# Optimization experiments

Measured on AMD Instinct MI355X. Metric: run time of the kernel, lower is better.

## Reference

```python
import jax, jax.numpy as jnp
import numpy as np

N_CTX = 4096
D_MODEL = 2048
D_HEAD = 128


def setup_inputs() -> dict:
    key = jax.random.key(0)
    k1, k2, k3, k4 = jax.random.split(key, 4)
    x = jax.random.normal(k1, (N_CTX, D_MODEL), dtype=jnp.float32)
    # torch nn.Linear weights are [out, in]; kept in that layout.
    Wk = jax.random.normal(k2, (D_HEAD, D_MODEL), dtype=jnp.float32) * (1.0 / np.sqrt(D_MODEL))
    Wq = jax.random.normal(k3, (D_HEAD, D_MODEL), dtype=jnp.float32) * (1.0 / np.sqrt(D_MODEL))
    W2 = jax.random.normal(k4, (D_MODEL, D_MODEL), dtype=jnp.float32) * (1.0 / np.sqrt(D_MODEL))
    return {"x": x, "Wk": Wk, "Wq": Wq, "W2": W2}


def reference(x, Wk, Wq, W2):
    # Faithful to the torch module: no 1/sqrt(d_head) scaling, V = x itself.
    n = x.shape[0]
    q = x @ Wq.T                     # [n, d_head]
    k = x @ Wk.T                     # [n, d_head]
    scores = q @ k.T                 # [n, n]
    # causal mask: strictly-upper-triangular entries -> -inf
    causal = jnp.tril(jnp.ones((n, n), dtype=bool))
    scores = jnp.where(causal, scores, -jnp.inf)
    attn = jax.nn.softmax(scores, axis=1)  # [n, n]
    out = attn @ x                   # [n, d_model] (V is the raw input)
    return out @ W2.T                # [n, d_model]
```

## Files before the change

### kernel.cpp

```cpp
#include <hip/hip_runtime.h>

#define NCTX 4096
#define DMODEL 2048
#define DHEAD 128

typedef _Float16 f16;
typedef f16 f16x8 __attribute__((ext_vector_type(8)));
typedef float f32x4 __attribute__((ext_vector_type(4)));
typedef unsigned short u16;

__device__ __forceinline__ u16 f2h(float f) {
  union { f16 h; u16 u; } v; v.h = (f16)f; return v.u;
}
__device__ __forceinline__ float h2f(u16 u) {
  union { u16 u; f16 h; } v; v.u = u; return (float)v.h;
}

__device__ __forceinline__ void gl_lds16(const void* g, void* l) {
  __builtin_amdgcn_global_load_lds((const __attribute__((address_space(1))) void*)g,
                                   (__attribute__((address_space(3))) void*)l, 16, 0, 0);
}

__device__ __forceinline__ void splitH4(float4 v, ushort4& h, ushort4& l) {
  h.x = f2h(v.x); l.x = f2h(v.x - h2f(h.x));
  h.y = f2h(v.y); l.y = f2h(v.y - h2f(h.y));
  h.z = f2h(v.z); l.z = f2h(v.z - h2f(h.z));
  h.w = f2h(v.w); l.w = f2h(v.w - h2f(h.w));
}

__global__ __launch_bounds__(256) void prep_all(const float* __restrict__ x,
                                                const float* __restrict__ Wq,
                                                const float* __restrict__ Wk,
                                                const float* __restrict__ W2,
                                                u16* __restrict__ xh, u16* __restrict__ xl,
                                                u16* __restrict__ Wf, u16* __restrict__ W2f,
                                                u16* __restrict__ XT) {
  __shared__ float tile[64][65];
  int b = blockIdx.x;
  int t = threadIdx.x;
  if (b < 2048) {
    int mb = (b >> 5) * 64, db = (b & 31) * 64;
    int tx = t & 15, ty = t >> 4;
#pragma unroll
    for (int rr = 0; rr < 4; ++rr) {
      int row = rr * 16 + ty;
      float4 v = *(const float4*)(x + (size_t)(mb + row) * DMODEL + db + tx * 4);
      ushort4 h, l; splitH4(v, h, l);
      size_t gi = ((size_t)(mb + row) * DMODEL + db) / 4 + tx;
      ((ushort4*)xh)[gi] = h; ((ushort4*)xl)[gi] = l;
      tile[row][tx * 4 + 0] = v.x; tile[row][tx * 4 + 1] = v.y;
      tile[row][tx * 4 + 2] = v.z; tile[row][tx * 4 + 3] = v.w;
    }
    __syncthreads();
#pragma unroll
    for (int rr = 0; rr < 4; ++rr) {
      int r = (t >> 4) * 4 + rr;
      int c0 = (t & 15) * 4;
      ushort4 o;
      o.x = f2h(tile[c0 + 0][r]); o.y = f2h(tile[c0 + 1][r]);
      o.z = f2h(tile[c0 + 2][r]); o.w = f2h(tile[c0 + 3][r]);
      *(ushort4*)(XT + (size_t)(db + r) * NCTX + mb + c0) = o;
    }
  } else if (b < 2560) {
    int wk = (b >= 2304);
    int i = (b - (wk ? 2304 : 2048)) * 256 + t;
    const float* W = wk ? Wk : Wq;
    size_t off = wk ? ((size_t)DHEAD * DMODEL / 4) : 0;
    float4 v = ((const float4*)W)[i];
    ushort4 o;
    o.x = f2h(v.x); o.y = f2h(v.y); o.z = f2h(v.z); o.w = f2h(v.w);
    ((ushort4*)Wf)[off + i] = o;
  } else {
    int i = (b - 2560) * 256 + t;
    float4 v = ((const float4*)W2)[i];
    ushort4 o;
    o.x = f2h(v.x); o.y = f2h(v.y); o.z = f2h(v.z); o.w = f2h(v.w);
    ((ushort4*)W2f)[i] = o;
  }
}

__global__ __launch_bounds__(256) void reduce8_f16(const float* __restrict__ P,
                                                   u16* __restrict__ out, int n4) {
  int i = blockIdx.x * 256 + threadIdx.x;
  if (i >= n4) return;
  float4 s = ((const float4*)P)[i];
#pragma unroll
  for (int z = 1; z < 8; ++z) {
    float4 v = ((const float4*)P)[(size_t)z * n4 + i];
    s.x += v.x; s.y += v.y; s.z += v.z; s.w += v.w;
  }
  ushort4 o;
  o.x = f2h(s.x); o.y = f2h(s.y); o.z = f2h(s.z); o.w = f2h(s.w);
  ((ushort4*)out)[i] = o;
}

__global__ __launch_bounds__(256) void reduce2_cast(const float* __restrict__ P0,
                                                    const float* __restrict__ P1,
                                                    u16* __restrict__ out,
                                                    int n4, int rowsplit4) {
  int i = blockIdx.x * 256 + threadIdx.x;
  if (i >= n4) return;
  float4 s = ((const float4*)P0)[i];
  if (i >= rowsplit4) {
    float4 v = ((const float4*)P1)[i];
    s.x += v.x; s.y += v.y; s.z += v.z; s.w += v.w;
  }
  ushort4 o;
  o.x = f2h(s.x); o.y = f2h(s.y); o.z = f2h(s.z); o.w = f2h(s.w);
  ((ushort4*)out)[i] = o;
}

__global__ __launch_bounds__(256) void reduce2_f32(const float* __restrict__ P0,
                                                   const float* __restrict__ P1,
                                                   float* __restrict__ out, int n4) {
  int i = blockIdx.x * 256 + threadIdx.x;
  if (i >= n4) return;
  float4 a = ((const float4*)P0)[i];
  float4 b = ((const float4*)P1)[i];
  a.x += b.x; a.y += b.y; a.z += b.z; a.w += b.w;
  ((float4*)out)[i] = a;
}

__global__ __launch_bounds__(256) void softmax_rows(const float* __restrict__ S,
                                                    u16* __restrict__ P) {
  int i = blockIdx.x;
  int t = threadIdx.x;
  __shared__ float rowbuf[NCTX];
  __shared__ float red[4];
  __shared__ float red2[4];
  const float* srow = S + (size_t)i * NCTX;
  int len = i + 1;
  int jmax = ((i >> 7) + 1) << 7;
  float mx = -3.0e38f;
  for (int j = t * 4; j < len; j += 1024) {
    if (j + 4 <= len) {
      float4 v = *(const float4*)(srow + j);
      *(float4*)(rowbuf + j) = v;
      mx = fmaxf(mx, fmaxf(fmaxf(v.x, v.y), fmaxf(v.z, v.w)));
    } else {
      for (int k = j; k < len; ++k) {
        float v = srow[k];
        rowbuf[k] = v;
        mx = fmaxf(mx, v);
      }
    }
  }
#pragma unroll
  for (int o = 32; o > 0; o >>= 1) mx = fmaxf(mx, __shfl_xor(mx, o, 64));
  if ((t & 63) == 0) red[t >> 6] = mx;
  __syncthreads();
  mx = fmaxf(fmaxf(red[0], red[1]), fmaxf(red[2], red[3]));
  float sum = 0.f;
  for (int j = t; j < len; j += 256) {
    float e = __expf(rowbuf[j] - mx);
    rowbuf[j] = e;
    sum += e;
  }
#pragma unroll
  for (int o = 32; o > 0; o >>= 1) sum += __shfl_xor(sum, o, 64);
  if ((t & 63) == 0) red2[t >> 6] = sum;
  __syncthreads();
  float inv = 1.0f / (red2[0] + red2[1] + red2[2] + red2[3]);
  u16* prow = P + (size_t)i * NCTX;
  for (int j = t * 4; j < jmax; j += 1024) {
    ushort4 o;
    o.x = (j + 0 < len) ? f2h(rowbuf[j + 0] * inv) : (u16)0;
    o.y = (j + 1 < len) ? f2h(rowbuf[j + 1] * inv) : (u16)0;
    o.z = (j + 2 < len) ? f2h(rowbuf[j + 2] * inv) : (u16)0;
    o.w = (j + 3 < len) ? f2h(rowbuf[j + 3] * inv) : (u16)0;
    *(ushort4*)(prow + j) = o;
  }
}

__global__ __launch_bounds__(256, 4) void gemm_f16_p(const u16* __restrict__ A,
                                                     const u16* __restrict__ B,
                                                     float* __restrict__ C,
                                                     int lda, int ldb, int ldc,
                                                     int K, int KC, size_t chunkStride,
                                                     int causal, int tri) {
  int bm = gridDim.x - 1 - blockIdx.x, bn = blockIdx.y, kc = blockIdx.z;
  if (tri && bn > bm) return;
  int kEnd = K;
  if (causal) { int ke = (bm + 1) * 128; if (ke < kEnd) kEnd = ke; }
  int kStart = kc * KC;
  if (kStart >= kEnd) return;
  int kStop = kStart + KC < kEnd ? kStart + KC : kEnd;
  __shared__ __align__(16) u16 As[128 * 64];
  __shared__ __align__(16) u16 Bs[128 * 64];
  int t = threadIdx.x;
  int lane = t & 63, w = t >> 6;
  int m0 = bm * 128, n0 = bn * 128;
  int wm = (w >> 1) * 64, wn = (w & 1) * 64;
  int mfrag = lane & 15, quad = lane >> 4;
  int srow = t >> 3, schunk = t & 7;
  int rsw = mfrag & 7;
  f32x4 acc[4][4] = {};
  for (int kt = kStart; kt < kStop; kt += 64) {
#pragma unroll
    for (int p = 0; p < 4; ++p) {
      int row = p * 32 + srow;
      int gsc = schunk ^ (row & 7);
      gl_lds16(A + (size_t)(m0 + row) * lda + kt + gsc * 8, As + (size_t)(p * 256 + t) * 8);
      gl_lds16(B + (size_t)(n0 + row) * ldb + kt + gsc * 8, Bs + (size_t)(p * 256 + t) * 8);
    }
    __syncthreads();
#pragma unroll
    for (int ks = 0; ks < 2; ++ks) {
      int c0 = ((ks * 4 + quad) ^ rsw) * 8;
      f16x8 af[4], bfr[4];
#pragma unroll
      for (int i = 0; i < 4; ++i)
        af[i] = *(const f16x8*)(As + (wm + i * 16 + mfrag) * 64 + c0);
#pragma unroll
      for (int j = 0; j < 4; ++j)
        bfr[j] = *(const f16x8*)(Bs + (wn + j * 16 + mfrag) * 64 + c0);
#pragma unroll
      for (int i = 0; i < 4; ++i)
#pragma unroll
        for (int j = 0; j < 4; ++j)
          acc[i][j] = __builtin_amdgcn_mfma_f32_16x16x32_f16(af[i], bfr[j], acc[i][j], 0, 0, 0);
    }
    __syncthreads();
  }
  float* Cc = C + (size_t)kc * chunkStride;
#pragma unroll
  for (int i = 0; i < 4; ++i)
#pragma unroll
    for (int j = 0; j < 4; ++j)
#pragma unroll
      for (int rr = 0; rr < 4; ++rr) {
        int row = m0 + wm + i * 16 + quad * 4 + rr;
        int col = n0 + wn + j * 16 + mfrag;
        Cc[(size_t)row * ldc + col] = acc[i][j][rr];
      }
}

__global__ __launch_bounds__(256, 3) void gemm_f16x2_p(const u16* __restrict__ Ah,
                                                       const u16* __restrict__ Al,
                                                       const u16* __restrict__ B,
                                                       float* __restrict__ C,
                                                       int lda, int ldb, int ldc,
                                                       int K, int KC, size_t chunkStride) {
  int bm = blockIdx.x, bn = blockIdx.y, kc = blockIdx.z;
  int kStart = kc * KC;
  int kStop = kStart + KC < K ? kStart + KC : K;
  __shared__ __align__(16) u16 Ash[128 * 64];
  __shared__ __align__(16) u16 Asl[128 * 64];
  __shared__ __align__(16) u16 Bs[128 * 64];
  int t = threadIdx.x;
  int lane = t & 63, w = t >> 6;
  int m0 = bm * 128, n0 = bn * 128;
  int wm = (w >> 1) * 64, wn = (w & 1) * 64;
  int mfrag = lane & 15, quad = lane >> 4;
  int srow = t >> 3, schunk = t & 7;
  int rsw = mfrag & 7;
  f32x4 acc[4][4] = {};
  for (int kt = kStart; kt < kStop; kt += 64) {
#pragma unroll
    for (int p = 0; p < 4; ++p) {
      int row = p * 32 + srow;
      int gsc = schunk ^ (row & 7);
      size_t aoff = (size_t)(m0 + row) * lda + kt + gsc * 8;
      size_t loff = (size_t)(p * 256 + t) * 8;
      gl_lds16(Ah + aoff, Ash + loff);
      gl_lds16(Al + aoff, Asl + loff);
      gl_lds16(B + (size_t)(n0 + row) * ldb + kt + gsc * 8, Bs + loff);
    }
    __syncthreads();
#pragma unroll
    for (int ks = 0; ks < 2; ++ks) {
      int c0 = ((ks * 4 + quad) ^ rsw) * 8;
      f16x8 a0[4], bfr[4];
#pragma unroll
      for (int j = 0; j < 4; ++j)
        bfr[j] = *(const f16x8*)(Bs + (wn + j * 16 + mfrag) * 64 + c0);
#pragma unroll
      for (int i = 0; i < 4; ++i)
        a0[i] = *(const f16x8*)(Ash + (wm + i * 16 + mfrag) * 64 + c0);
#pragma unroll
      for (int i = 0; i < 4; ++i)
#pragma unroll
        for (int j = 0; j < 4; ++j)
          acc[i][j] = __builtin_amdgcn_mfma_f32_16x16x32_f16(a0[i], bfr[j], acc[i][j], 0, 0, 0);
#pragma unroll
      for (int i = 0; i < 4; ++i)
        a0[i] = *(const f16x8*)(Asl + (wm + i * 16 + mfrag) * 64 + c0);
#pragma unroll
      for (int i = 0; i < 4; ++i)
#pragma unroll
        for (int j = 0; j < 4; ++j)
          acc[i][j] = __builtin_amdgcn_mfma_f32_16x16x32_f16(a0[i], bfr[j], acc[i][j], 0, 0, 0);
    }
    __syncthreads();
  }
  float* Cc = C + (size_t)kc * chunkStride;
#pragma unroll
  for (int i = 0; i < 4; ++i)
#pragma unroll
    for (int j = 0; j < 4; ++j)
#pragma unroll
      for (int rr = 0; rr < 4; ++rr) {
        int row = m0 + wm + i * 16 + quad * 4 + rr;
        int col = n0 + wn + j * 16 + mfrag;
        Cc[(size_t)row * ldc + col] = acc[i][j][rr];
      }
}

extern "C" void kernel_launch(void* const* d_in, const int* in_sizes, int n_in,
                              void* d_out, int out_size, void* d_ws, size_t ws_size,
                              hipStream_t stream) {
  const float* x  = (const float*)d_in[0];
  const float* Wk = (const float*)d_in[1];
  const float* Wq = (const float*)d_in[2];
  const float* W2 = (const float*)d_in[3];

  char* ws = (char*)d_ws;
  const size_t MB = 1024 * 1024;
  u16*   QKf  = (u16*)  (ws + 0);
  u16*   Wf   = (u16*)  (ws + 2 * MB);
  u16*   xT   = (u16*)  (ws + 3 * MB);
  u16*   W2f  = (u16*)  (ws + 19 * MB);
  u16*   outb = (u16*)  (ws + 27 * MB);
  u16*   attn = (u16*)  (ws + 43 * MB);
  u16*   xh   = (u16*)  (ws + 75 * MB);
  u16*   xl   = (u16*)  (ws + 91 * MB);
  float* QKp  = (float*)(ws + 107 * MB);
  float* S    = (float*)(ws + 75 * MB);
  float* P0   = (float*)(ws + 75 * MB);
  float* P1   = (float*)(ws + 107 * MB);

  const int XN4 = NCTX * DMODEL / 4;
  const int QKN4 = NCTX * 256 / 4;

  prep_all<<<6656, 256, 0, stream>>>(x, Wq, Wk, W2, xh, xl, Wf, W2f, xT);

  gemm_f16x2_p<<<dim3(NCTX / 128, 2, 8), 256, 0, stream>>>(
      xh, xl, Wf, QKp, DMODEL, DMODEL, 256, DMODEL, 256, (size_t)NCTX * 256);
  reduce8_f16<<<(QKN4 + 255) / 256, 256, 0, stream>>>(QKp, QKf, QKN4);

  gemm_f16_p<<<dim3(NCTX / 128, NCTX / 128, 1), 256, 0, stream>>>(
      QKf, QKf + DHEAD, S, 256, 256, NCTX, DHEAD, DHEAD, 0, 0, 1);
  softmax_rows<<<NCTX, 256, 0, stream>>>(S, attn);

  gemm_f16_p<<<dim3(NCTX / 128, DMODEL / 128, 2), 256, 0, stream>>>(
      attn, xT, P0, NCTX, NCTX, DMODEL, NCTX, 2048, (size_t)NCTX * DMODEL, 1, 0);
  reduce2_cast<<<(XN4 + 255) / 256, 256, 0, stream>>>(P0, P1, outb, XN4,
                                                      2048 * 2048 / 4);

  gemm_f16_p<<<dim3(NCTX / 128, DMODEL / 128, 2), 256, 0, stream>>>(
      outb, W2f, P0, DMODEL, DMODEL, DMODEL, DMODEL, 1024, (size_t)NCTX * DMODEL, 0, 0);
  reduce2_f32<<<(XN4 + 255) / 256, 256, 0, stream>>>(P0, P1, (float*)d_out, XN4);
}
```

Before: 270.2 us.

## Store split-K GEMM partials in fp16 and use causal four-way K split

Adds a GEMM variant that writes split-K partial sums as fp16 rather than fp32, which halves partial-buffer traffic for the attn@x and out@W2 stages. The attn@x GEMM now uses a four-way K split with causal early exit and reversed row order so the heaviest tiles start first. A row-aware reducer sums only the chunks that exist for each row. The cost is reduced precision in the partial sums, since each fp16 partial is rounded before accumulation.

```diff
diff --git a/kernel.cpp b/kernel.cpp
--- a/kernel.cpp
+++ b/kernel.cpp
@@ -8,6 +8,7 @@
 typedef f16 f16x8 __attribute__((ext_vector_type(8)));
 typedef float f32x4 __attribute__((ext_vector_type(4)));
 typedef unsigned short u16;
+typedef u16 u16x8 __attribute__((ext_vector_type(8)));
 
 __device__ __forceinline__ u16 f2h(float f) {
   union { f16 h; u16 u; } v; v.h = (f16)f; return v.u;
@@ -94,31 +95,38 @@
   ((ushort4*)out)[i] = o;
 }
 
-__global__ __launch_bounds__(256) void reduce2_cast(const float* __restrict__ P0,
-                                                    const float* __restrict__ P1,
-                                                    u16* __restrict__ out,
-                                                    int n4, int rowsplit4) {
+__global__ __launch_bounds__(256) void reduce_c4(const u16* __restrict__ P,
+                                                 u16* __restrict__ out, size_t cs) {
+  int row = blockIdx.x;
+  int t = threadIdx.x;
+  int nc = (row >> 10) + 1;
+  size_t base = (size_t)row * DMODEL + t * 8;
+  float s[8] = {};
+  for (int c = 0; c < nc; ++c) {
+    u16x8 v = *(const u16x8*)(P + (size_t)c * cs + base);
+#pragma unroll
+    for (int k = 0; k < 8; ++k) s[k] += h2f(v[k]);
+  }
+  u16x8 o;
+#pragma unroll
+  for (int k = 0; k < 8; ++k) o[k] = f2h(s[k]);
+  *(u16x8*)(out + base) = o;
+}
+
+__global__ __launch_bounds__(256) void reduce2_hf(const u16* __restrict__ P0,
+                                                  const u16* __restrict__ P1,
+                                                  float* __restrict__ out, int n8) {
   int i = blockIdx.x * 256 + threadIdx.x;
-  if (i >= n4) return;
-  float4 s = ((const float4*)P0)[i];
-  if (i >= rowsplit4) {
-    float4 v = ((const float4*)P1)[i];
-    s.x += v.x; s.y += v.y; s.z += v.z; s.w += v.w;
-  }
-  ushort4 o;
-  o.x = f2h(s.x); o.y = f2h(s.y); o.z = f2h(s.z); o.w = f2h(s.w);
-  ((ushort4*)out)[i] = o;
-}
-
-__global__ __launch_bounds__(256) void reduce2_f32(const float* __restrict__ P0,
-                                                   const float* __restrict__ P1,
-                                                   float* __restrict__ out, int n4) {
-  int i = blockIdx.x * 256 + threadIdx.x;
-  if (i >= n4) return;
-  float4 a = ((const float4*)P0)[i];
-  float4 b = ((const float4*)P1)[i];
-  a.x += b.x; a.y += b.y; a.z += b.z; a.w += b.w;
-  ((float4*)out)[i] = a;
+  if (i >= n8) return;
+  u16x8 a = ((const u16x8*)P0)[i];
+  u16x8 b = ((const u16x8*)P1)[i];
+  float4 o0, o1;
+  o0.x = h2f(a[0]) + h2f(b[0]); o0.y = h2f(a[1]) + h2f(b[1]);
+  o0.z = h2f(a[2]) + h2f(b[2]); o0.w = h2f(a[3]) + h2f(b[3]);
+  o1.x = h2f(a[4]) + h2f(b[4]); o1.y = h2f(a[5]) + h2f(b[5]);
+  o1.z = h2f(a[6]) + h2f(b[6]); o1.w = h2f(a[7]) + h2f(b[7]);
+  ((float4*)out)[i * 2 + 0] = o0;
+  ((float4*)out)[i * 2 + 1] = o1;
 }
 
 __global__ __launch_bounds__(256) void softmax_rows(const float* __restrict__ S,
@@ -235,6 +243,68 @@
       }
 }
 
+__global__ __launch_bounds__(256, 4) void gemm_f16_h(const u16* __restrict__ A,
+                                                     const u16* __restrict__ B,
+                                                     u16* __restrict__ C,
+                                                     int lda, int ldb, int ldc,
+                                                     int K, int KC, size_t chunkStride,
+                                                     int causal) {
+  int bm = gridDim.x - 1 - blockIdx.x, bn = blockIdx.y, kc = blockIdx.z;
+  int kEnd = K;
+  if (causal) { int ke = (bm + 1) * 128; if (ke < kEnd) kEnd = ke; }
+  int kStart = kc * KC;
+  if (kStart >= kEnd) return;
+  int kStop = kStart + KC < kEnd ? kStart + KC : kEnd;
+  __shared__ __align__(16) u16 As[128 * 64];
+  __shared__ __align__(16) u16 Bs[128 * 64];
+  int t = threadIdx.x;
+  int lane = t & 63, w = t >> 6;
+  int m0 = bm * 128, n0 = bn * 128;
+  int wm = (w >> 1) * 64, wn = (w & 1) * 64;
+  int mfrag = lane & 15, quad = lane >> 4;
+  int srow = t >> 3, schunk = t & 7;
+  int rsw = mfrag & 7;
+  f32x4 acc[4][4] = {};
+  for (int kt = kStart; kt < kStop; kt += 64) {
+#pragma unroll
+    for (int p = 0; p < 4; ++p) {
+      int row = p * 32 + srow;
+      int gsc = schunk ^ (row & 7);
+      gl_lds16(A + (size_t)(m0 + row) * lda + kt + gsc * 8, As + (size_t)(p * 256 + t) * 8);
+      gl_lds16(B + (size_t)(n0 + row) * ldb + kt + gsc * 8, Bs + (size_t)(p * 256 + t) * 8);
+    }
+    __syncthreads();
+#pragma unroll
+    for (int ks = 0; ks < 2; ++ks) {
+      int c0 = ((ks * 4 + quad) ^ rsw) * 8;
+      f16x8 af[4], bfr[4];
+#pragma unroll
+      for (int i = 0; i < 4; ++i)
+        af[i] = *(const f16x8*)(As + (wm + i * 16 + mfrag) * 64 + c0);
+#pragma unroll
+      for (int j = 0; j < 4; ++j)
+        bfr[j] = *(const f16x8*)(Bs + (wn + j * 16 + mfrag) * 64 + c0);
+#pragma unroll
+      for (int i = 0; i < 4; ++i)
+#pragma unroll
+        for (int j = 0; j < 4; ++j)
+          acc[i][j] = __builtin_amdgcn_mfma_f32_16x16x32_f16(af[i], bfr[j], acc[i][j], 0, 0, 0);
+    }
+    __syncthreads();
+  }
+  u16* Cc = C + (size_t)kc * chunkStride;
+#pragma unroll
+  for (int i = 0; i < 4; ++i)
+#pragma unroll
+    for (int j = 0; j < 4; ++j)
+#pragma unroll
+      for (int rr = 0; rr < 4; ++rr) {
+        int row = m0 + wm + i * 16 + quad * 4 + rr;
+        int col = n0 + wn + j * 16 + mfrag;
+        Cc[(size_t)row * ldc + col] = f2h(acc[i][j][rr]);
+      }
+}
+
 __global__ __launch_bounds__(256, 3) void gemm_f16x2_p(const u16* __restrict__ Ah,
                                                        const u16* __restrict__ Al,
                                                        const u16* __restrict__ B,
@@ -326,11 +396,11 @@
   u16*   xl   = (u16*)  (ws + 91 * MB);
   float* QKp  = (float*)(ws + 107 * MB);
   float* S    = (float*)(ws + 75 * MB);
-  float* P0   = (float*)(ws + 75 * MB);
-  float* P1   = (float*)(ws + 107 * MB);
-
-  const int XN4 = NCTX * DMODEL / 4;
+  u16*   Ph   = (u16*)  (ws + 75 * MB);
+
+  const int XN8 = NCTX * DMODEL / 8;
   const int QKN4 = NCTX * 256 / 4;
+  const size_t CS = (size_t)NCTX * DMODEL;
 
   prep_all<<<6656, 256, 0, stream>>>(x, Wq, Wk, W2, xh, xl, Wf, W2f, xT);
 
@@ -342,12 +412,11 @@
       QKf, QKf + DHEAD, S, 256, 256, NCTX, DHEAD, DHEAD, 0, 0, 1);
   softmax_rows<<<NCTX, 256, 0, stream>>>(S, attn);
 
-  gemm_f16_p<<<dim3(NCTX / 128, DMODEL / 128, 2), 256, 0, stream>>>(
-      attn, xT, P0, NCTX, NCTX, DMODEL, NCTX, 2048, (size_t)NCTX * DMODEL, 1, 0);
-  reduce2_cast<<<(XN4 + 255) / 256, 256, 0, stream>>>(P0, P1, outb, XN4,
-                                                      2048 * 2048 / 4);
-
-  gemm_f16_p<<<dim3(NCTX / 128, DMODEL / 128, 2), 256, 0, stream>>>(
-      outb, W2f, P0, DMODEL, DMODEL, DMODEL, DMODEL, 1024, (size_t)NCTX * DMODEL, 0, 0);
-  reduce2_f32<<<(XN4 + 255) / 256, 256, 0, stream>>>(P0, P1, (float*)d_out, XN4);
-}
+  gemm_f16_h<<<dim3(NCTX / 128, DMODEL / 128, 4), 256, 0, stream>>>(
+      attn, xT, Ph, NCTX, NCTX, DMODEL, NCTX, 1024, CS, 1);
+  reduce_c4<<<NCTX, 256, 0, stream>>>(Ph, outb, CS);
+
+  gemm_f16_h<<<dim3(NCTX / 128, DMODEL / 128, 2), 256, 0, stream>>>(
+      outb, W2f, Ph, DMODEL, DMODEL, DMODEL, DMODEL, 1024, CS, 0);
+  reduce2_hf<<<(XN8 + 255) / 256, 256, 0, stream>>>(Ph, Ph + CS, (float*)d_out, XN8);
+}
```

New measurement: 271.4 us. No clear change (+0.5%).
